# Performance work log

Measured on AMD Instinct MI355X. Metric: run time of the kernel, lower is better.

## Reference

```python
import jax, jax.numpy as jnp
import numpy as np

NUM_VERTS = 6890
NUM_FACES = 13776
H, W = 1024, 1024
N, D = 16, 3


def setup_inputs() -> dict:
    key = jax.random.key(0)
    k1, k2, k3, k4, k5 = jax.random.split(key, 5)
    verts_attr = jax.random.normal(k1, (N, NUM_VERTS, D), dtype=jnp.float32)
    face_tensor = jax.random.randint(k2, (NUM_FACES, 3), 0, NUM_VERTS, dtype=jnp.int64)
    pix = jax.random.randint(k3, (H, W), 0, NUM_FACES, dtype=jnp.int64)
    bg = jax.random.uniform(k4, (H, W)) < 0.1
    pix_to_face = jnp.where(bg, jnp.int64(-1), pix)
    # barycentric coords on the simplex
    b = jax.random.uniform(k5, (H, W, 3), dtype=jnp.float32) + 1e-6
    bary_coords = b / jnp.sum(b, axis=-1, keepdims=True)
    return {
        'verts_attr': verts_attr,
        'face_tensor': face_tensor,
        'pix_to_face': pix_to_face,
        'bary_coords': bary_coords,
    }


def reference(verts_attr, face_tensor, pix_to_face, bary_coords):
    n, v, d = verts_attr.shape
    flat = verts_attr.reshape(n * v, d)  # packed (N*V, D)
    # NOTE: original uses (NUM_VERTS - 1) as the per-batch offset (replicated faithfully)
    offsets = (jnp.arange(n, dtype=jnp.int64) * (v - 1))[:, None, None]
    faces_packed = (face_tensor[None] + offsets).reshape(-1, 3)  # (N*F, 3)
    face_attr = flat[faces_packed]  # (N*F, 3, D)
    # NOTE: original repeats pix_to_face across batch without per-batch face offset,
    # so all batches gather from batch-0 face attributes (replicated faithfully).
    mask = pix_to_face >= 0  # (H, W)
    idx = jnp.where(mask, pix_to_face, 0)
    pix_attr = face_attr[idx]  # (H, W, 3, D)
    out_hw = jnp.einsum('hwk,hwkd->hwd', bary_coords, pix_attr)
    out_hw = jnp.where(mask[..., None], out_hw, jnp.zeros((), out_hw.dtype))
    maps_padded = jnp.broadcast_to(out_hw[None], (n,) + out_hw.shape)  # (N, H, W, D)
    return maps_padded
```

## Files before the change

### kernel.cpp

```cpp
#include <hip/hip_runtime.h>
#include <hip/hip_bf16.h>

constexpr int HH    = 1024;
constexpr int WW    = 1024;
constexpr int NPIX  = HH * WW;
constexpr int NB    = 16;
constexpr int PPT   = 8;
constexpr int BLOCK = 256;

__global__ __launch_bounds__(BLOCK) void uv_render_kernel(
    const float* __restrict__ verts,
    const int*   __restrict__ faces,
    const int*   __restrict__ p2f,
    const float* __restrict__ bary,
    float*       __restrict__ out)
{
    const int  t  = blockIdx.x * blockDim.x + threadIdx.x;
    const long p0 = (long)t * PPT;
    if (p0 >= NPIX) return;

    const int4* pf4 = (const int4*)(p2f + p0);
    const int4 f01 = pf4[0];
    const int4 f23 = pf4[1];
    const int fidx[PPT] = {f01.x, f01.y, f01.z, f01.w, f23.x, f23.y, f23.z, f23.w};

    const float4* b4 = (const float4*)(bary + p0 * 3);
    float b[PPT * 3];
    #pragma unroll
    for (int i = 0; i < 6; ++i) {
        const float4 v = b4[i];
        b[4 * i + 0] = v.x;
        b[4 * i + 1] = v.y;
        b[4 * i + 2] = v.z;
        b[4 * i + 3] = v.w;
    }

    alignas(16) float res[PPT * 3];
    #pragma unroll
    for (int i = 0; i < PPT; ++i) {
        const int f = fidx[i];
        float o0 = 0.f, o1 = 0.f, o2 = 0.f;
        if (f >= 0) {
            const int v0 = faces[3 * f + 0];
            const int v1 = faces[3 * f + 1];
            const int v2 = faces[3 * f + 2];
            const float* a0 = verts + 3 * v0;
            const float* a1 = verts + 3 * v1;
            const float* a2 = verts + 3 * v2;
            const float w0 = b[3 * i + 0];
            const float w1 = b[3 * i + 1];
            const float w2 = b[3 * i + 2];
            o0 = w0 * a0[0] + w1 * a1[0] + w2 * a2[0];
            o1 = w0 * a0[1] + w1 * a1[1] + w2 * a2[1];
            o2 = w0 * a0[2] + w1 * a1[2] + w2 * a2[2];
        }
        res[3 * i + 0] = o0;
        res[3 * i + 1] = o1;
        res[3 * i + 2] = o2;
    }

    const float4* r4 = (const float4*)res;
    const float4 r0 = r4[0], r1 = r4[1], r2 = r4[2];
    const float4 r3 = r4[3], r4v = r4[4], r5 = r4[5];
    #pragma unroll
    for (int n = 0; n < NB; ++n) {
        float4* dst = (float4*)(out + (size_t)n * (size_t)NPIX * 3 + p0 * 3);
        dst[0] = r0;
        dst[1] = r1;
        dst[2] = r2;
        dst[3] = r3;
        dst[4] = r4v;
        dst[5] = r5;
    }
}

extern "C" void kernel_launch(void* const* d_in, const int* in_sizes, int n_in,
                              void* d_out, int out_size, void* d_ws, size_t ws_size,
                              hipStream_t stream) {
    const float* verts = (const float*)d_in[0];
    const int*   faces = (const int*)d_in[1];
    const int*   p2f   = (const int*)d_in[2];
    const float* bary  = (const float*)d_in[3];
    float*       out   = (float*)d_out;

    const int threads = NPIX / PPT;
    const int grid    = threads / BLOCK;
    uv_render_kernel<<<grid, BLOCK, 0, stream>>>(verts, faces, p2f, bary, out);
}
```

Before: 245.4 us.

## Split render into compute-map kernel and separate broadcast-replicate kernel

Splits the single kernel in two. The first computes the interpolated map once into batch slot 0, with 4 pixels per thread. The second reads that map back and writes it to the other 15 batch slots with fully coalesced float4 stores. The aim is to separate the latency-bound gather from the bandwidth-bound 16x broadcast write. The cost is an extra launch plus a 12 MB reread of the map.

```diff
diff --git a/kernel.cpp b/kernel.cpp
--- a/kernel.cpp
+++ b/kernel.cpp
@@ -5,35 +5,29 @@
 constexpr int WW    = 1024;
 constexpr int NPIX  = HH * WW;
 constexpr int NB    = 16;
-constexpr int PPT   = 8;
+constexpr int PPT   = 4;
 constexpr int BLOCK = 256;
+constexpr int MAPF4 = NPIX * 3 / 4;
 
-__global__ __launch_bounds__(BLOCK) void uv_render_kernel(
+__global__ __launch_bounds__(BLOCK) void uv_compute_map(
     const float* __restrict__ verts,
     const int*   __restrict__ faces,
     const int*   __restrict__ p2f,
     const float* __restrict__ bary,
     float*       __restrict__ out)
 {
-    const int  t  = blockIdx.x * blockDim.x + threadIdx.x;
-    const long p0 = (long)t * PPT;
+    const int t  = blockIdx.x * blockDim.x + threadIdx.x;
+    const int p0 = t * PPT;
     if (p0 >= NPIX) return;
 
-    const int4* pf4 = (const int4*)(p2f + p0);
-    const int4 f01 = pf4[0];
-    const int4 f23 = pf4[1];
-    const int fidx[PPT] = {f01.x, f01.y, f01.z, f01.w, f23.x, f23.y, f23.z, f23.w};
+    const int4 fi = *(const int4*)(p2f + p0);
+    const int fidx[PPT] = {fi.x, fi.y, fi.z, fi.w};
 
-    const float4* b4 = (const float4*)(bary + p0 * 3);
-    float b[PPT * 3];
-    #pragma unroll
-    for (int i = 0; i < 6; ++i) {
-        const float4 v = b4[i];
-        b[4 * i + 0] = v.x;
-        b[4 * i + 1] = v.y;
-        b[4 * i + 2] = v.z;
-        b[4 * i + 3] = v.w;
-    }
+    const float4* b4 = (const float4*)(bary + (size_t)p0 * 3);
+    const float4 bv0 = b4[0], bv1 = b4[1], bv2 = b4[2];
+    const float b[PPT * 3] = {bv0.x, bv0.y, bv0.z, bv0.w,
+                              bv1.x, bv1.y, bv1.z, bv1.w,
+                              bv2.x, bv2.y, bv2.z, bv2.w};
 
     alignas(16) float res[PPT * 3];
     #pragma unroll
@@ -59,19 +53,23 @@
         res[3 * i + 2] = o2;
     }
 
+    float4* dst = (float4*)(out + (size_t)p0 * 3);
     const float4* r4 = (const float4*)res;
-    const float4 r0 = r4[0], r1 = r4[1], r2 = r4[2];
-    const float4 r3 = r4[3], r4v = r4[4], r5 = r4[5];
+    dst[0] = r4[0];
+    dst[1] = r4[1];
+    dst[2] = r4[2];
+}
+
+__global__ __launch_bounds__(BLOCK) void uv_replicate(
+    float* __restrict__ out)
+{
+    const int tid = blockIdx.x * blockDim.x + threadIdx.x;
+    if (tid >= MAPF4) return;
+    const float4 v = ((const float4*)out)[tid];
+    float4* o4 = (float4*)out;
     #pragma unroll
-    for (int n = 0; n < NB; ++n) {
-        float4* dst = (float4*)(out + (size_t)n * (size_t)NPIX * 3 + p0 * 3);
-        dst[0] = r0;
-        dst[1] = r1;
-        dst[2] = r2;
-        dst[3] = r3;
-        dst[4] = r4v;
-        dst[5] = r5;
-    }
+    for (int n = 1; n < NB; ++n)
+        o4[(size_t)n * MAPF4 + tid] = v;
 }
 
 extern "C" void kernel_launch(void* const* d_in, const int* in_sizes, int n_in,
@@ -83,7 +81,9 @@
     const float* bary  = (const float*)d_in[3];
     float*       out   = (float*)d_out;
 
-    const int threads = NPIX / PPT;
-    const int grid    = threads / BLOCK;
-    uv_render_kernel<<<grid, BLOCK, 0, stream>>>(verts, faces, p2f, bary, out);
+    const int grid1 = NPIX / PPT / BLOCK;
+    uv_compute_map<<<grid1, BLOCK, 0, stream>>>(verts, faces, p2f, bary, out);
+
+    const int grid2 = MAPF4 / BLOCK;
+    uv_replicate<<<grid2, BLOCK, 0, stream>>>(out);
 }
```

Result: faster. 230.0 us (-6.3%).
